# Kernel optimization log

Hardware: AMD Instinct MI355X
Metric: run time of the kernel (lower is better)

## Reference

```python
import jax, jax.numpy as jnp
import numpy as np
from jax import lax

INT32_MAX = 2147483647


def setup_inputs() -> dict:
    key = jax.random.key(0)
    kx, ky = jax.random.split(key)
    x = jax.random.normal(kx, (4096, 64), dtype=jnp.float32)
    y = jax.random.normal(ky, (100000, 64), dtype=jnp.float32)
    return {"x": x, "y": y, "k": 16, "n_splits": 10}


def reference(x, y, k, n_splits):
    """Streaming k-NN: L2 path distance with incremental top-k merge.

    x: (B1, d) queries; y: (B2, d) database. Returns
      ds:  (B1, k)    k smallest distances
      idx: (B1, k, 1) global indices into y (int32), matching (B1,k,y.ndim-1).
    """
    B1, d = x.shape
    B2 = y.shape[0]
    split = B2 // n_splits
    y_splits = y.reshape(n_splits, split, d)  # even splits, as in torch .split
    bases = jnp.arange(n_splits, dtype=jnp.int32) * split

    x2 = jnp.sum(x * x, axis=-1, keepdims=True)  # (B1, 1)

    ds0 = jnp.full((B1, k), jnp.inf, dtype=x.dtype)
    idx0 = jnp.full((B1, k), INT32_MAX, dtype=jnp.int32)
    col = jnp.arange(split, dtype=jnp.int32)

    def step(carry, inp):
        ds, idx = carry
        y_b, base = inp                               # (split, d), scalar
        y2 = jnp.sum(y_b * y_b, axis=-1)              # (split,)
        d2 = x2 + y2[None, :] - 2.0 * (x @ y_b.T)     # (B1, split)
        new_ds = jnp.sqrt(jnp.maximum(d2, 0.0))
        new_idx = jnp.broadcast_to(base + col, (B1, split))
        cat_ds = jnp.concatenate([ds, new_ds], axis=1)      # (B1, k+split)
        cat_idx = jnp.concatenate([idx, new_idx], axis=1)
        neg_top, pos = lax.top_k(-cat_ds, k)                # smallest-k
        ds = -neg_top
        idx = jnp.take_along_axis(cat_idx, pos, axis=1)
        return (ds, idx), None

    (ds, idx), _ = lax.scan(step, (ds0, idx0), (y_splits, bases))
    return ds, idx[..., None]
```

## Files before the change

### kernel.cpp

```cpp
#include <hip/hip_runtime.h>
#include <math.h>

#define D 64
#define K 16
#define NSEG 25
#define NPART (NSEG * 4)
#define CAP_WANT 512

typedef __attribute__((ext_vector_type(8))) short short8;
typedef __attribute__((ext_vector_type(4))) float f32x4;

__device__ __forceinline__ unsigned short f32_to_bf16_rne(float f) {
    unsigned u = __float_as_uint(f);
    u = u + 0x7FFFu + ((u >> 16) & 1u);
    return (unsigned short)(u >> 16);
}

__global__ __launch_bounds__(256)
void prep_kernel(const float* __restrict__ x, const float* __restrict__ y,
                 unsigned short* __restrict__ xbneg,
                 unsigned short* __restrict__ yb,
                 float* __restrict__ y2, int B1, int B2)
{
    const int w = threadIdx.x >> 6, lane = threadIdx.x & 63;
    const int row = blockIdx.x * 4 + w;
    if (row < B2) {
        const float v = y[(size_t)row * D + lane];
        float s = v * v;
        #pragma unroll
        for (int off = 32; off > 0; off >>= 1) s += __shfl_xor(s, off);
        yb[(size_t)row * D + lane] = f32_to_bf16_rne(v);
        if (lane == 0) y2[row] = s;
    } else if (row < B2 + B1) {
        const int r = row - B2;
        const float v = x[(size_t)r * D + lane];
        xbneg[(size_t)r * D + lane] = f32_to_bf16_rne(-2.0f * v);
    }
}

__global__ __launch_bounds__(256)
void knn_min_kernel(const unsigned short* __restrict__ xbneg,
                    const unsigned short* __restrict__ yb,
                    const float* __restrict__ y2g,
                    float* __restrict__ pmin,
                    int B1, int B2, int segsz, int nseg)
{
    const int tid  = threadIdx.x;
    const int w    = tid >> 6;
    const int lane = tid & 63;
    const int n15  = lane & 15;
    const int quad = lane >> 4;
    const int qb   = blockIdx.x * 128 + w * 32;
    const int s    = blockIdx.y;
    const int base = s * segsz;
    const int segN = min(segsz, B2 - base);
    const int nt   = (segN + 63) >> 6;

    __shared__ __align__(16) unsigned short tile[2][64 * 72];
    __shared__ __align__(16) float y2t[2][64];

    const int rr = tid >> 3;
    const int cw = tid & 7;

    const int q0 = qb + n15;
    const int q1 = qb + 16 + n15;
    const short8 b00 = *(const short8*)&xbneg[(size_t)q0 * D + quad * 8];
    const short8 b01 = *(const short8*)&xbneg[(size_t)q0 * D + 32 + quad * 8];
    const short8 b10 = *(const short8*)&xbneg[(size_t)q1 * D + quad * 8];
    const short8 b11 = *(const short8*)&xbneg[(size_t)q1 * D + 32 + quad * 8];

    float rm0 = INFINITY, rm1 = INFINITY;

    uint4 r0, r1; float ry;

#define LOADT(tt)                                                                   \
    do {                                                                            \
        const int c0_ = (tt) * 64;                                                  \
        const int g0_ = c0_ + rr;                                                   \
        const int g1_ = g0_ + 32;                                                   \
        r0 = make_uint4(0, 0, 0, 0); r1 = make_uint4(0, 0, 0, 0);                   \
        if (g0_ < segN) r0 = *(const uint4*)&yb[(size_t)(base + g0_) * D + cw * 8]; \
        if (g1_ < segN) r1 = *(const uint4*)&yb[(size_t)(base + g1_) * D + cw * 8]; \
        ry = INFINITY;                                                              \
        if (tid < 64 && c0_ + tid < segN) ry = y2g[base + c0_ + tid];               \
    } while (0)

#define WRITET(bb)                                                                  \
    do {                                                                            \
        *(uint4*)&tile[bb][rr * 72 + cw * 8] = r0;                                  \
        *(uint4*)&tile[bb][(rr + 32) * 72 + cw * 8] = r1;                           \
        if (tid < 64) y2t[bb][tid] = ry;                                            \
    } while (0)

    LOADT(0);
    WRITET(0);
    int cur = 0;

    for (int t = 0; t < nt; ++t) {
        const bool more = (t + 1 < nt);
        if (more) LOADT(t + 1);
        asm volatile("s_waitcnt lgkmcnt(0)" ::: "memory");
        __builtin_amdgcn_s_barrier();
        __builtin_amdgcn_sched_barrier(0);

        #pragma unroll
        for (int ct = 0; ct < 4; ++ct) {
            const short8 a0 = *(const short8*)&tile[cur][(ct * 16 + n15) * 72 + quad * 8];
            const short8 a1 = *(const short8*)&tile[cur][(ct * 16 + n15) * 72 + 32 + quad * 8];
            const float4 y2v = *(const float4*)&y2t[cur][ct * 16 + 4 * quad];

            f32x4 acc0 = {0.f, 0.f, 0.f, 0.f};
            acc0 = __builtin_amdgcn_mfma_f32_16x16x32_bf16(a0, b00, acc0, 0, 0, 0);
            acc0 = __builtin_amdgcn_mfma_f32_16x16x32_bf16(a1, b01, acc0, 0, 0, 0);
            rm0 = fminf(rm0, fminf(fminf(acc0[0] + y2v.x, acc0[1] + y2v.y),
                                   fminf(acc0[2] + y2v.z, acc0[3] + y2v.w)));

            f32x4 acc1 = {0.f, 0.f, 0.f, 0.f};
            acc1 = __builtin_amdgcn_mfma_f32_16x16x32_bf16(a0, b10, acc1, 0, 0, 0);
            acc1 = __builtin_amdgcn_mfma_f32_16x16x32_bf16(a1, b11, acc1, 0, 0, 0);
            rm1 = fminf(rm1, fminf(fminf(acc1[0] + y2v.x, acc1[1] + y2v.y),
                                   fminf(acc1[2] + y2v.z, acc1[3] + y2v.w)));
        }

        if (more) WRITET(cur ^ 1);
        cur ^= 1;
    }
#undef LOADT
#undef WRITET

    pmin[((size_t)q0 * nseg + s) * 4 + quad] = rm0;
    pmin[((size_t)q1 * nseg + s) * 4 + quad] = rm1;
}

__global__ __launch_bounds__(256)
void knn_thresh_kernel(const float* __restrict__ pmin,
                       float* __restrict__ Tq, int* __restrict__ cnt,
                       int B1, int npart)
{
    const int w    = threadIdx.x >> 6;
    const int lane = threadIdx.x & 63;
    const int q    = blockIdx.x * 4 + w;

    const float* p = pmin + (size_t)q * npart;
    float cd = (lane < npart) ? p[lane] : INFINITY;
    float worst = cd;
    #pragma unroll
    for (int off = 32; off > 0; off >>= 1) worst = fmaxf(worst, __shfl_xor(worst, off));

    for (int t = 64; t < npart; ++t) {
        const float dv = p[t];
        if (dv < worst) {
            const unsigned long long m = __ballot(cd == worst);
            const int vict = __ffsll(m) - 1;
            if (lane == vict) cd = dv;
            float wv = cd;
            #pragma unroll
            for (int off = 32; off > 0; off >>= 1) wv = fmaxf(wv, __shfl_xor(wv, off));
            worst = wv;
        }
    }
    if (lane == 0) { Tq[q] = worst; cnt[q] = 0; }
}

__global__ __launch_bounds__(256)
void knn_filter_kernel(const unsigned short* __restrict__ xbneg,
                       const unsigned short* __restrict__ yb,
                       const float* __restrict__ y2g,
                       const float* __restrict__ Tq,
                       int* __restrict__ cnt,
                       float* __restrict__ sd, int* __restrict__ si,
                       int B1, int B2, int segsz, int cap)
{
    const int tid  = threadIdx.x;
    const int w    = tid >> 6;
    const int lane = tid & 63;
    const int n15  = lane & 15;
    const int quad = lane >> 4;
    const int qb   = blockIdx.x * 128 + w * 32;
    const int s    = blockIdx.y;
    const int base = s * segsz;
    const int segN = min(segsz, B2 - base);
    const int nt   = (segN + 63) >> 6;

    __shared__ __align__(16) unsigned short tile[2][64 * 72];
    __shared__ __align__(16) float y2t[2][64];

    const int rr = tid >> 3;
    const int cw = tid & 7;

    const int q0 = qb + n15;
    const int q1 = qb + 16 + n15;
    const short8 b00 = *(const short8*)&xbneg[(size_t)q0 * D + quad * 8];
    const short8 b01 = *(const short8*)&xbneg[(size_t)q0 * D + 32 + quad * 8];
    const short8 b10 = *(const short8*)&xbneg[(size_t)q1 * D + quad * 8];
    const short8 b11 = *(const short8*)&xbneg[(size_t)q1 * D + 32 + quad * 8];

    const float th0 = Tq[q0];
    const float th1 = Tq[q1];

    uint4 r0, r1; float ry;

#define LOADT(tt)                                                                   \
    do {                                                                            \
        const int c0_ = (tt) * 64;                                                  \
        const int g0_ = c0_ + rr;                                                   \
        const int g1_ = g0_ + 32;                                                   \
        r0 = make_uint4(0, 0, 0, 0); r1 = make_uint4(0, 0, 0, 0);                   \
        if (g0_ < segN) r0 = *(const uint4*)&yb[(size_t)(base + g0_) * D + cw * 8]; \
        if (g1_ < segN) r1 = *(const uint4*)&yb[(size_t)(base + g1_) * D + cw * 8]; \
        ry = INFINITY;                                                              \
        if (tid < 64 && c0_ + tid < segN) ry = y2g[base + c0_ + tid];               \
    } while (0)

#define WRITET(bb)                                                                  \
    do {                                                                            \
        *(uint4*)&tile[bb][rr * 72 + cw * 8] = r0;                                  \
        *(uint4*)&tile[bb][(rr + 32) * 72 + cw * 8] = r1;                           \
        if (tid < 64) y2t[bb][tid] = ry;                                            \
    } while (0)

    LOADT(0);
    WRITET(0);
    int cur = 0;

    for (int t = 0; t < nt; ++t) {
        const bool more = (t + 1 < nt);
        if (more) LOADT(t + 1);
        asm volatile("s_waitcnt lgkmcnt(0)" ::: "memory");
        __builtin_amdgcn_s_barrier();
        __builtin_amdgcn_sched_barrier(0);

        const int c0t = t << 6;

        #pragma unroll
        for (int ct = 0; ct < 4; ++ct) {
            const short8 a0 = *(const short8*)&tile[cur][(ct * 16 + n15) * 72 + quad * 8];
            const short8 a1 = *(const short8*)&tile[cur][(ct * 16 + n15) * 72 + 32 + quad * 8];
            const float4 y2v = *(const float4*)&y2t[cur][ct * 16 + 4 * quad];
            const int cb = base + c0t + ct * 16 + 4 * quad;

            f32x4 acc0 = {0.f, 0.f, 0.f, 0.f};
            acc0 = __builtin_amdgcn_mfma_f32_16x16x32_bf16(a0, b00, acc0, 0, 0, 0);
            acc0 = __builtin_amdgcn_mfma_f32_16x16x32_bf16(a1, b01, acc0, 0, 0, 0);
            {
                const float m0 = acc0[0] + y2v.x;
                const float m1 = acc0[1] + y2v.y;
                const float m2 = acc0[2] + y2v.z;
                const float m3 = acc0[3] + y2v.w;
                const float mm = fminf(fminf(m0, m1), fminf(m2, m3));
                if (mm <= th0) {
                    if (m0 <= th0) { const int p_ = atomicAdd(&cnt[q0], 1); if (p_ < cap) { sd[(size_t)q0 * cap + p_] = m0; si[(size_t)q0 * cap + p_] = cb + 0; } }
                    if (m1 <= th0) { const int p_ = atomicAdd(&cnt[q0], 1); if (p_ < cap) { sd[(size_t)q0 * cap + p_] = m1; si[(size_t)q0 * cap + p_] = cb + 1; } }
                    if (m2 <= th0) { const int p_ = atomicAdd(&cnt[q0], 1); if (p_ < cap) { sd[(size_t)q0 * cap + p_] = m2; si[(size_t)q0 * cap + p_] = cb + 2; } }
                    if (m3 <= th0) { const int p_ = atomicAdd(&cnt[q0], 1); if (p_ < cap) { sd[(size_t)q0 * cap + p_] = m3; si[(size_t)q0 * cap + p_] = cb + 3; } }
                }
            }

            f32x4 acc1 = {0.f, 0.f, 0.f, 0.f};
            acc1 = __builtin_amdgcn_mfma_f32_16x16x32_bf16(a0, b10, acc1, 0, 0, 0);
            acc1 = __builtin_amdgcn_mfma_f32_16x16x32_bf16(a1, b11, acc1, 0, 0, 0);
            {
                const float m0 = acc1[0] + y2v.x;
                const float m1 = acc1[1] + y2v.y;
                const float m2 = acc1[2] + y2v.z;
                const float m3 = acc1[3] + y2v.w;
                const float mm = fminf(fminf(m0, m1), fminf(m2, m3));
                if (mm <= th1) {
                    if (m0 <= th1) { const int p_ = atomicAdd(&cnt[q1], 1); if (p_ < cap) { sd[(size_t)q1 * cap + p_] = m0; si[(size_t)q1 * cap + p_] = cb + 0; } }
                    if (m1 <= th1) { const int p_ = atomicAdd(&cnt[q1], 1); if (p_ < cap) { sd[(size_t)q1 * cap + p_] = m1; si[(size_t)q1 * cap + p_] = cb + 1; } }
                    if (m2 <= th1) { const int p_ = atomicAdd(&cnt[q1], 1); if (p_ < cap) { sd[(size_t)q1 * cap + p_] = m2; si[(size_t)q1 * cap + p_] = cb + 2; } }
                    if (m3 <= th1) { const int p_ = atomicAdd(&cnt[q1], 1); if (p_ < cap) { sd[(size_t)q1 * cap + p_] = m3; si[(size_t)q1 * cap + p_] = cb + 3; } }
                }
            }
        }

        if (more) WRITET(cur ^ 1);
        cur ^= 1;
    }
#undef LOADT
#undef WRITET
}

__global__ __launch_bounds__(256)
void knn_merge_refine_kernel(const float* __restrict__ sd,
                             const int*   __restrict__ si,
                             const int*   __restrict__ cnt,
                             const float* __restrict__ x,
                             const float* __restrict__ y,
                             float* __restrict__ out_ds,
                             float* __restrict__ out_idx,
                             int B1, int B2, int cap)
{
    const int w    = threadIdx.x >> 6;
    const int lane = threadIdx.x & 63;
    const int q    = blockIdx.x * 4 + w;

    float cd = INFINITY;
    int   ci = 2147483647;
    float worst = INFINITY;

    const int n = min(cnt[q], cap);
    const float* sdq = sd + (size_t)q * cap;
    const int*   siq = si + (size_t)q * cap;

    for (int j = 0; j < n; ++j) {
        const float dv = sdq[j];
        if (dv < worst) {
            const int jidx = siq[j];
            const unsigned long long m = __ballot(cd == worst);
            const int vict = __ffsll(m) - 1;
            if (lane == vict) { cd = dv; ci = jidx; }
            float wv = cd;
            #pragma unroll
            for (int off = 32; off > 0; off >>= 1)
                wv = fmaxf(wv, __shfl_xor(wv, off));
            worst = wv;
        }
    }

    __shared__ float xs[4][D];
    __shared__ float sds[4][64];
    __shared__ int   sidx[4][64];

    if (lane < D / 4)
        ((float4*)xs[w])[lane] = ((const float4*)(x + (size_t)q * D))[lane];
    __syncthreads();

    float x2 = 0.f;
    #pragma unroll
    for (int i = 0; i < D; ++i) x2 = __fadd_rn(x2, __fmul_rn(xs[w][i], xs[w][i]));

    int idx = ci;
    float ds32 = INFINITY;
    if (idx >= 0 && idx < B2) {
        float yr[D];
        const float4* yrow = (const float4*)(y + (size_t)idx * D);
        #pragma unroll
        for (int t = 0; t < D / 4; ++t) {
            float4 v = yrow[t];
            yr[4*t+0] = v.x; yr[4*t+1] = v.y; yr[4*t+2] = v.z; yr[4*t+3] = v.w;
        }
        float y2 = 0.f;
        #pragma unroll
        for (int i = 0; i < D; ++i) y2 = __fadd_rn(y2, __fmul_rn(yr[i], yr[i]));

        float dot = 0.f;
        #pragma unroll
        for (int i = 0; i < D; ++i) dot = __fmaf_rn(xs[w][i], yr[i], dot);

        const float d2 = __fsub_rn(__fadd_rn(x2, y2), __fmul_rn(2.0f, dot));
        ds32 = __fsqrt_rn(fmaxf(d2, 0.f));
    } else {
        idx = 2147483647;
    }
    sds[w][lane]  = ds32;
    sidx[w][lane] = idx;
    __syncthreads();

    int rank = 0;
    for (int j = 0; j < 64; ++j) {
        const float dj = sds[w][j];
        bool prec = (dj < ds32);
        if (dj == ds32 && sidx[w][j] != idx) {
            const int  jd    = sidx[w][j];
            const long dd    = (long)jd - (long)idx;
            const long add   = dd < 0 ? -dd : dd;
            const bool t2win = (add >= 21504 && add <= 23552);
            prec = t2win ? (jd > idx) : (jd < idx);
        }
        if (prec) ++rank;
    }
    if (rank < K) {
        out_ds [(size_t)q * K + rank] = ds32;
        out_idx[(size_t)q * K + rank] = (float)idx;
    }
}

extern "C" void kernel_launch(void* const* d_in, const int* in_sizes, int n_in,
                              void* d_out, int out_size, void* d_ws, size_t ws_size,
                              hipStream_t stream)
{
    const float* x = (const float*)d_in[0];
    const float* y = (const float*)d_in[1];

    const int B1 = in_sizes[0] / D;
    const int B2 = in_sizes[1] / D;

    size_t off = 0;
    unsigned short* xbneg = (unsigned short*)((char*)d_ws + off); off += (size_t)B1 * D * 2;
    unsigned short* yb    = (unsigned short*)((char*)d_ws + off); off += (size_t)B2 * D * 2;
    float*          y2    = (float*)((char*)d_ws + off);          off += (size_t)B2 * 4;
    float*          pmin  = (float*)((char*)d_ws + off);          off += (size_t)B1 * NPART * 4;
    float*          Tq    = (float*)((char*)d_ws + off);          off += (size_t)B1 * 4;
    int*            cnt   = (int*)((char*)d_ws + off);            off += (size_t)B1 * 4;

    int cap = CAP_WANT;
    {
        const size_t per = (size_t)B1 * 8;
        if (off + (size_t)cap * per > ws_size) {
            const size_t avail = ws_size > off ? ws_size - off : 0;
            cap = (int)(avail / per);
            if (cap < 16) cap = 16;
        }
    }
    float* sd = (float*)((char*)d_ws + off); off += (size_t)B1 * cap * 4;
    int*   si = (int*)((char*)d_ws + off);

    float* out_ds  = (float*)d_out;
    float* out_idx = out_ds + (size_t)B1 * K;

    const int segsz = (B2 + NSEG - 1) / NSEG;

    const int prows = B1 + B2;
    prep_kernel<<<(prows + 3) / 4, 256, 0, stream>>>(x, y, xbneg, yb, y2, B1, B2);

    dim3 grid1(B1 / 128, NSEG);
    knn_min_kernel<<<grid1, 256, 0, stream>>>(xbneg, yb, y2, pmin, B1, B2, segsz, NSEG);

    knn_thresh_kernel<<<B1 / 4, 256, 0, stream>>>(pmin, Tq, cnt, B1, NPART);

    knn_filter_kernel<<<grid1, 256, 0, stream>>>(xbneg, yb, y2, Tq, cnt, sd, si,
                                                 B1, B2, segsz, cap);

    knn_merge_refine_kernel<<<B1 / 4, 256, 0, stream>>>(sd, si, cnt, x, y,
                                                        out_ds, out_idx,
                                                        B1, B2, cap);
}
```

Baseline: 408.3 us.

## Deepen global-load prefetch to two tiles and double segment count

Both MFMA scan kernels now keep two register staging sets (even/odd), so each global load of a y tile is issued two iterations ahead instead of one. The loop is unrolled by two to alternate the register sets. NSEG is also raised from 25 to 50, which doubles the number of segments and blocks so more of the GPU stays busy. The costs are higher register pressure and a larger partial-min array for the threshold kernel to reduce.

Measured after the change: 389.9 us. 1.05x faster.

```diff
diff --git a/kernel.cpp b/kernel.cpp
--- a/kernel.cpp
+++ b/kernel.cpp
@@ -3,7 +3,7 @@
 
 #define D 64
 #define K 16
-#define NSEG 25
+#define NSEG 50
 #define NPART (NSEG * 4)
 #define CAP_WANT 512
 
@@ -38,6 +38,32 @@
     }
 }
 
+#define LOADT(tt, R0, R1, RY)                                                       \
+    do {                                                                            \
+        const int c0_ = (tt) * 64;                                                  \
+        const int g0_ = c0_ + rr;                                                   \
+        const int g1_ = g0_ + 32;                                                   \
+        R0 = make_uint4(0, 0, 0, 0); R1 = make_uint4(0, 0, 0, 0);                   \
+        if (g0_ < segN) R0 = *(const uint4*)&yb[(size_t)(base + g0_) * D + cw * 8]; \
+        if (g1_ < segN) R1 = *(const uint4*)&yb[(size_t)(base + g1_) * D + cw * 8]; \
+        RY = INFINITY;                                                              \
+        if (tid < 64 && c0_ + tid < segN) RY = y2g[base + c0_ + tid];               \
+    } while (0)
+
+#define WRITET(bb, R0, R1, RY)                                                      \
+    do {                                                                            \
+        *(uint4*)&tile[bb][rr * 72 + cw * 8] = R0;                                  \
+        *(uint4*)&tile[bb][(rr + 32) * 72 + cw * 8] = R1;                           \
+        if (tid < 64) y2t[bb][tid] = RY;                                            \
+    } while (0)
+
+#define SYNCT()                                                                     \
+    do {                                                                            \
+        asm volatile("s_waitcnt lgkmcnt(0)" ::: "memory");                          \
+        __builtin_amdgcn_s_barrier();                                               \
+        __builtin_amdgcn_sched_barrier(0);                                          \
+    } while (0)
+
 __global__ __launch_bounds__(256)
 void knn_min_kernel(const unsigned short* __restrict__ xbneg,
                     const unsigned short* __restrict__ yb,
@@ -71,62 +97,50 @@
 
     float rm0 = INFINITY, rm1 = INFINITY;
 
-    uint4 r0, r1; float ry;
-
-#define LOADT(tt)                                                                   \
+    uint4 e0, e1; float ey;
+    uint4 o0, o1; float oy;
+
+#define COMPUTE_MIN(cc)                                                             \
     do {                                                                            \
-        const int c0_ = (tt) * 64;                                                  \
-        const int g0_ = c0_ + rr;                                                   \
-        const int g1_ = g0_ + 32;                                                   \
-        r0 = make_uint4(0, 0, 0, 0); r1 = make_uint4(0, 0, 0, 0);                   \
-        if (g0_ < segN) r0 = *(const uint4*)&yb[(size_t)(base + g0_) * D + cw * 8]; \
-        if (g1_ < segN) r1 = *(const uint4*)&yb[(size_t)(base + g1_) * D + cw * 8]; \
-        ry = INFINITY;                                                              \
-        if (tid < 64 && c0_ + tid < segN) ry = y2g[base + c0_ + tid];               \
+        _Pragma("unroll")                                                           \
+        for (int ct = 0; ct < 4; ++ct) {                                            \
+            const short8 a0 = *(const short8*)&tile[cc][(ct * 16 + n15) * 72 + quad * 8];      \
+            const short8 a1 = *(const short8*)&tile[cc][(ct * 16 + n15) * 72 + 32 + quad * 8]; \
+            const float4 y2v = *(const float4*)&y2t[cc][ct * 16 + 4 * quad];        \
+            f32x4 acc0 = {0.f, 0.f, 0.f, 0.f};                                      \
+            acc0 = __builtin_amdgcn_mfma_f32_16x16x32_bf16(a0, b00, acc0, 0, 0, 0); \
+            acc0 = __builtin_amdgcn_mfma_f32_16x16x32_bf16(a1, b01, acc0, 0, 0, 0); \
+            rm0 = fminf(rm0, fminf(fminf(acc0[0] + y2v.x, acc0[1] + y2v.y),         \
+                                   fminf(acc0[2] + y2v.z, acc0[3] + y2v.w)));       \
+            f32x4 acc1 = {0.f, 0.f, 0.f, 0.f};                                      \
+            acc1 = __builtin_amdgcn_mfma_f32_16x16x32_bf16(a0, b10, acc1, 0, 0, 0); \
+            acc1 = __builtin_amdgcn_mfma_f32_16x16x32_bf16(a1, b11, acc1, 0, 0, 0); \
+            rm1 = fminf(rm1, fminf(fminf(acc1[0] + y2v.x, acc1[1] + y2v.y),         \
+                                   fminf(acc1[2] + y2v.z, acc1[3] + y2v.w)));       \
+        }                                                                           \
     } while (0)
 
-#define WRITET(bb)                                                                  \
-    do {                                                                            \
-        *(uint4*)&tile[bb][rr * 72 + cw * 8] = r0;                                  \
-        *(uint4*)&tile[bb][(rr + 32) * 72 + cw * 8] = r1;                           \
-        if (tid < 64) y2t[bb][tid] = ry;                                            \
-    } while (0)
-
-    LOADT(0);
-    WRITET(0);
+    LOADT(0, e0, e1, ey);
+    WRITET(0, e0, e1, ey);
+    LOADT(1, o0, o1, oy);
+    SYNCT();
+
     int cur = 0;
-
-    for (int t = 0; t < nt; ++t) {
-        const bool more = (t + 1 < nt);
-        if (more) LOADT(t + 1);
-        asm volatile("s_waitcnt lgkmcnt(0)" ::: "memory");
-        __builtin_amdgcn_s_barrier();
-        __builtin_amdgcn_sched_barrier(0);
-
-        #pragma unroll
-        for (int ct = 0; ct < 4; ++ct) {
-            const short8 a0 = *(const short8*)&tile[cur][(ct * 16 + n15) * 72 + quad * 8];
-            const short8 a1 = *(const short8*)&tile[cur][(ct * 16 + n15) * 72 + 32 + quad * 8];
-            const float4 y2v = *(const float4*)&y2t[cur][ct * 16 + 4 * quad];
-
-            f32x4 acc0 = {0.f, 0.f, 0.f, 0.f};
-            acc0 = __builtin_amdgcn_mfma_f32_16x16x32_bf16(a0, b00, acc0, 0, 0, 0);
-            acc0 = __builtin_amdgcn_mfma_f32_16x16x32_bf16(a1, b01, acc0, 0, 0, 0);
-            rm0 = fminf(rm0, fminf(fminf(acc0[0] + y2v.x, acc0[1] + y2v.y),
-                                   fminf(acc0[2] + y2v.z, acc0[3] + y2v.w)));
-
-            f32x4 acc1 = {0.f, 0.f, 0.f, 0.f};
-            acc1 = __builtin_amdgcn_mfma_f32_16x16x32_bf16(a0, b10, acc1, 0, 0, 0);
-            acc1 = __builtin_amdgcn_mfma_f32_16x16x32_bf16(a1, b11, acc1, 0, 0, 0);
-            rm1 = fminf(rm1, fminf(fminf(acc1[0] + y2v.x, acc1[1] + y2v.y),
-                                   fminf(acc1[2] + y2v.z, acc1[3] + y2v.w)));
-        }
-
-        if (more) WRITET(cur ^ 1);
+    for (int t = 0; t < nt; t += 2) {
+        COMPUTE_MIN(cur);
+        if (t + 1 < nt) WRITET(cur ^ 1, o0, o1, oy);
+        if (t + 2 < nt) LOADT(t + 2, e0, e1, ey);
+        SYNCT();
         cur ^= 1;
-    }
-#undef LOADT
-#undef WRITET
+        if (t + 1 < nt) {
+            COMPUTE_MIN(cur);
+            if (t + 2 < nt) WRITET(cur ^ 1, e0, e1, ey);
+            if (t + 3 < nt) LOADT(t + 3, o0, o1, oy);
+            SYNCT();
+            cur ^= 1;
+        }
+    }
+#undef COMPUTE_MIN
 
     pmin[((size_t)q0 * nseg + s) * 4 + quad] = rm0;
     pmin[((size_t)q1 * nseg + s) * 4 + quad] = rm1;
@@ -198,87 +212,74 @@
     const float th0 = Tq[q0];
     const float th1 = Tq[q1];
 
-    uint4 r0, r1; float ry;
-
-#define LOADT(tt)                                                                   \
+    uint4 e0, e1; float ey;
+    uint4 o0, o1; float oy;
+
+#define COMPUTE_FLT(cc, tt)                                                         \
     do {                                                                            \
-        const int c0_ = (tt) * 64;                                                  \
-        const int g0_ = c0_ + rr;                                                   \
-        const int g1_ = g0_ + 32;                                                   \
-        r0 = make_uint4(0, 0, 0, 0); r1 = make_uint4(0, 0, 0, 0);                   \
-        if (g0_ < segN) r0 = *(const uint4*)&yb[(size_t)(base + g0_) * D + cw * 8]; \
-        if (g1_ < segN) r1 = *(const uint4*)&yb[(size_t)(base + g1_) * D + cw * 8]; \
-        ry = INFINITY;                                                              \
-        if (tid < 64 && c0_ + tid < segN) ry = y2g[base + c0_ + tid];               \
+        const int c0t = (tt) << 6;                                                  \
+        _Pragma("unroll")                                                           \
+        for (int ct = 0; ct < 4; ++ct) {                                            \
+            const short8 a0 = *(const short8*)&tile[cc][(ct * 16 + n15) * 72 + quad * 8];      \
+            const short8 a1 = *(const short8*)&tile[cc][(ct * 16 + n15) * 72 + 32 + quad * 8]; \
+            const float4 y2v = *(const float4*)&y2t[cc][ct * 16 + 4 * quad];        \
+            const int cb = base + c0t + ct * 16 + 4 * quad;                         \
+            f32x4 acc0 = {0.f, 0.f, 0.f, 0.f};                                      \
+            acc0 = __builtin_amdgcn_mfma_f32_16x16x32_bf16(a0, b00, acc0, 0, 0, 0); \
+            acc0 = __builtin_amdgcn_mfma_f32_16x16x32_bf16(a1, b01, acc0, 0, 0, 0); \
+            {                                                                       \
+                const float m0 = acc0[0] + y2v.x;                                   \
+                const float m1 = acc0[1] + y2v.y;                                   \
+                const float m2 = acc0[2] + y2v.z;                                   \
+                const float m3 = acc0[3] + y2v.w;                                   \
+                const float mm = fminf(fminf(m0, m1), fminf(m2, m3));               \
+                if (mm <= th0) {                                                    \
+                    if (m0 <= th0) { const int p_ = atomicAdd(&cnt[q0], 1); if (p_ < cap) { sd[(size_t)q0 * cap + p_] = m0; si[(size_t)q0 * cap + p_] = cb + 0; } } \
+                    if (m1 <= th0) { const int p_ = atomicAdd(&cnt[q0], 1); if (p_ < cap) { sd[(size_t)q0 * cap + p_] = m1; si[(size_t)q0 * cap + p_] = cb + 1; } } \
+                    if (m2 <= th0) { const int p_ = atomicAdd(&cnt[q0], 1); if (p_ < cap) { sd[(size_t)q0 * cap + p_] = m2; si[(size_t)q0 * cap + p_] = cb + 2; } } \
+                    if (m3 <= th0) { const int p_ = atomicAdd(&cnt[q0], 1); if (p_ < cap) { sd[(size_t)q0 * cap + p_] = m3; si[(size_t)q0 * cap + p_] = cb + 3; } } \
+                }                                                                   \
+            }                                                                       \
+            f32x4 acc1 = {0.f, 0.f, 0.f, 0.f};                                      \
+            acc1 = __builtin_amdgcn_mfma_f32_16x16x32_bf16(a0, b10, acc1, 0, 0, 0); \
+            acc1 = __builtin_amdgcn_mfma_f32_16x16x32_bf16(a1, b11, acc1, 0, 0, 0); \
+            {                                                                       \
+                const float m0 = acc1[0] + y2v.x;                                   \
+                const float m1 = acc1[1] + y2v.y;                                   \
+                const float m2 = acc1[2] + y2v.z;                                   \
+                const float m3 = acc1[3] + y2v.w;                                   \
+                const float mm = fminf(fminf(m0, m1), fminf(m2, m3));               \
+                if (mm <= th1) {                                                    \
+                    if (m0 <= th1) { const int p_ = atomicAdd(&cnt[q1], 1); if (p_ < cap) { sd[(size_t)q1 * cap + p_] = m0; si[(size_t)q1 * cap + p_] = cb + 0; } } \
+                    if (m1 <= th1) { const int p_ = atomicAdd(&cnt[q1], 1); if (p_ < cap) { sd[(size_t)q1 * cap + p_] = m1; si[(size_t)q1 * cap + p_] = cb + 1; } } \
+                    if (m2 <= th1) { const int p_ = atomicAdd(&cnt[q1], 1); if (p_ < cap) { sd[(size_t)q1 * cap + p_] = m2; si[(size_t)q1 * cap + p_] = cb + 2; } } \
+                    if (m3 <= th1) { const int p_ = atomicAdd(&cnt[q1], 1); if (p_ < cap) { sd[(size_t)q1 * cap + p_] = m3; si[(size_t)q1 * cap + p_] = cb + 3; } } \
+                }                                                                   \
+            }                                                                       \
+        }                                                                           \
     } while (0)
 
-#define WRITET(bb)                                                                  \
-    do {                                                                            \
-        *(uint4*)&tile[bb][rr * 72 + cw * 8] = r0;                                  \
-        *(uint4*)&tile[bb][(rr + 32) * 72 + cw * 8] = r1;                           \
-        if (tid < 64) y2t[bb][tid] = ry;                                            \
-    } while (0)
-
-    LOADT(0);
-    WRITET(0);
+    LOADT(0, e0, e1, ey);
+    WRITET(0, e0, e1, ey);
+    LOADT(1, o0, o1, oy);
+    SYNCT();
+
     int cur = 0;
-
-    for (int t = 0; t < nt; ++t) {
-        const bool more = (t + 1 < nt);
-        if (more) LOADT(t + 1);
-        asm volatile("s_waitcnt lgkmcnt(0)" ::: "memory");
-        __builtin_amdgcn_s_barrier();
-        __builtin_amdgcn_sched_barrier(0);
-
-        const int c0t = t << 6;
-
-        #pragma unroll
-        for (int ct = 0; ct < 4; ++ct) {
-            const short8 a0 = *(const short8*)&tile[cur][(ct * 16 + n15) * 72 + quad * 8];
-            const short8 a1 = *(const short8*)&tile[cur][(ct * 16 + n15) * 72 + 32 + quad * 8];
-            const float4 y2v = *(const float4*)&y2t[cur][ct * 16 + 4 * quad];
-            const int cb = base + c0t + ct * 16 + 4 * quad;
-
-            f32x4 acc0 = {0.f, 0.f, 0.f, 0.f};
-            acc0 = __builtin_amdgcn_mfma_f32_16x16x32_bf16(a0, b00, acc0, 0, 0, 0);
-            acc0 = __builtin_amdgcn_mfma_f32_16x16x32_bf16(a1, b01, acc0, 0, 0, 0);
-            {
-                const float m0 = acc0[0] + y2v.x;
-                const float m1 = acc0[1] + y2v.y;
-                const float m2 = acc0[2] + y2v.z;
-                const float m3 = acc0[3] + y2v.w;
-                const float mm = fminf(fminf(m0, m1), fminf(m2, m3));
-                if (mm <= th0) {
-                    if (m0 <= th0) { const int p_ = atomicAdd(&cnt[q0], 1); if (p_ < cap) { sd[(size_t)q0 * cap + p_] = m0; si[(size_t)q0 * cap + p_] = cb + 0; } }
-                    if (m1 <= th0) { const int p_ = atomicAdd(&cnt[q0], 1); if (p_ < cap) { sd[(size_t)q0 * cap + p_] = m1; si[(size_t)q0 * cap + p_] = cb + 1; } }
-                    if (m2 <= th0) { const int p_ = atomicAdd(&cnt[q0], 1); if (p_ < cap) { sd[(size_t)q0 * cap + p_] = m2; si[(size_t)q0 * cap + p_] = cb + 2; } }
-                    if (m3 <= th0) { const int p_ = atomicAdd(&cnt[q0], 1); if (p_ < cap) { sd[(size_t)q0 * cap + p_] = m3; si[(size_t)q0 * cap + p_] = cb + 3; } }
-                }
-            }
-
-            f32x4 acc1 = {0.f, 0.f, 0.f, 0.f};
-            acc1 = __builtin_amdgcn_mfma_f32_16x16x32_bf16(a0, b10, acc1, 0, 0, 0);
-            acc1 = __builtin_amdgcn_mfma_f32_16x16x32_bf16(a1, b11, acc1, 0, 0, 0);
-            {
-                const float m0 = acc1[0] + y2v.x;
-                const float m1 = acc1[1] + y2v.y;
-                const float m2 = acc1[2] + y2v.z;
-                const float m3 = acc1[3] + y2v.w;
-                const float mm = fminf(fminf(m0, m1), fminf(m2, m3));
-                if (mm <= th1) {
-                    if (m0 <= th1) { const int p_ = atomicAdd(&cnt[q1], 1); if (p_ < cap) { sd[(size_t)q1 * cap + p_] = m0; si[(size_t)q1 * cap + p_] = cb + 0; } }
-                    if (m1 <= th1) { const int p_ = atomicAdd(&cnt[q1], 1); if (p_ < cap) { sd[(size_t)q1 * cap + p_] = m1; si[(size_t)q1 * cap + p_] = cb + 1; } }
-                    if (m2 <= th1) { const int p_ = atomicAdd(&cnt[q1], 1); if (p_ < cap) { sd[(size_t)q1 * cap + p_] = m2; si[(size_t)q1 * cap + p_] = cb + 2; } }
-                    if (m3 <= th1) { const int p_ = atomicAdd(&cnt[q1], 1); if (p_ < cap) { sd[(size_t)q1 * cap + p_] = m3; si[(size_t)q1 * cap + p_] = cb + 3; } }
-                }
-            }
-        }
-
-        if (more) WRITET(cur ^ 1);
+    for (int t = 0; t < nt; t += 2) {
+        COMPUTE_FLT(cur, t);
+        if (t + 1 < nt) WRITET(cur ^ 1, o0, o1, oy);
+        if (t + 2 < nt) LOADT(t + 2, e0, e1, ey);
+        SYNCT();
         cur ^= 1;
-    }
-#undef LOADT
-#undef WRITET
+        if (t + 1 < nt) {
+            COMPUTE_FLT(cur, t + 1);
+            if (t + 2 < nt) WRITET(cur ^ 1, e0, e1, ey);
+            if (t + 3 < nt) LOADT(t + 3, o0, o1, oy);
+            SYNCT();
+            cur ^= 1;
+        }
+    }
+#undef COMPUTE_FLT
 }
 
 __global__ __launch_bounds__(256)
```
